# Performance work log

Hardware: AMD Instinct MI355X
Metric: run time of the kernel (lower is better)

Reference implementation:

```python
import jax, jax.numpy as jnp
import numpy as np

VOCAB = 64
H = 64
B, L = 256, 2048


def setup_inputs() -> dict:
    key = jax.random.key(0)
    ks = jax.random.split(key, 12)
    s = 0.02
    return {
        "seq":   jax.random.randint(ks[0], (B, L), 0, VOCAB),
        "embed": jax.random.normal(ks[1], (VOCAB, H), jnp.float32) * s,
        "W1":    jax.random.normal(ks[2], (H, 2 * H), jnp.float32) * s,
        "b1":    jnp.zeros((2 * H,), jnp.float32),
        "W2":    jax.random.normal(ks[3], (2 * H, H), jnp.float32) * s,
        "b2":    jnp.zeros((H,), jnp.float32),
        "gamma": jnp.ones((H,), jnp.float32),
        "beta":  jnp.zeros((H,), jnp.float32),
        "Wr":    jax.random.normal(ks[4], (H, H), jnp.float32) * s,
        "br":    jnp.zeros((H,), jnp.float32),
        "Wo":    jax.random.normal(ks[5], (H, VOCAB), jnp.float32) * s,
        "bo":    jnp.zeros((VOCAB,), jnp.float32),
    }


def _layernorm(x, gamma, beta, eps=1e-5):
    mu = x.mean(-1, keepdims=True)
    var = ((x - mu) ** 2).mean(-1, keepdims=True)
    return (x - mu) * jax.lax.rsqrt(var + eps) * gamma + beta


def _encode(seq, embed, W1, b1, W2, b2, gamma, beta):
    h = embed[seq]                                   # [B, L, H]
    ff = jax.nn.relu(h @ W1 + b1) @ W2 + b2
    return _layernorm(h + ff, gamma, beta)


def _run_memory(hidden):
    # sequential energy-gated delta-rule update of fast-weight M [B,H,H]
    Bd, Ld, Hd = hidden.shape
    M0 = jnp.zeros((Bd, Hd, Hd), hidden.dtype)

    def step(carry, k):
        M, writes = carry
        v = k                                        # k == v == hidden[:, t]
        v_pred = jnp.einsum('bij,bj->bi', M, k)
        denom = (k * k).sum(-1, keepdims=True) + 1e-6
        delta_v = v - v_pred / denom
        dM = delta_v[:, :, None] * k[:, None, :]     # outer product [B,H,H]
        E_before = -0.5 * (M * M).sum((-2, -1))
        Mn = M + dM
        E_after = -0.5 * (Mn * Mn).sum((-2, -1))
        gate = E_after < E_before                    # [B] bool
        M = jnp.where(gate[:, None, None], Mn, M)
        writes = writes + gate.sum().astype(jnp.float32)
        return (M, writes), None

    keys = jnp.swapaxes(hidden[:, :-1, :], 0, 1)     # [L-1, B, H]
    (M, writes), _ = jax.lax.scan(step, (M0, jnp.float32(0.0)), keys)
    return M, writes


def reference(seq, embed, W1, b1, W2, b2, gamma, beta, Wr, br, Wo, bo):
    hidden = _encode(seq, embed, W1, b1, W2, b2, gamma, beta)
    Bd, Ld, Hd = hidden.shape
    M, writes = _run_memory(hidden)
    write_rate = writes / jnp.float32(Bd * (Ld - 1))
    query = hidden[:, -1, :]
    ctx = jnp.einsum('bij,bj->bi', M, query)
    logits = (ctx @ Wr + br) @ Wo + bo               # [B, VOCAB]
    return logits, write_rate
```

## Files before the change

### kernel.cpp

```cpp
#include <hip/hip_runtime.h>
#include <math.h>

#define VOCAB 64
#define H 64
#define BB 256
#define LL 2048

__device__ __forceinline__ float wave_sum_dpp(float x) {
  int t;
  float r = x;
  t = __builtin_amdgcn_update_dpp(0, __float_as_int(r), 0x111, 0xf, 0xf, true); r += __int_as_float(t);
  t = __builtin_amdgcn_update_dpp(0, __float_as_int(r), 0x112, 0xf, 0xf, true); r += __int_as_float(t);
  t = __builtin_amdgcn_update_dpp(0, __float_as_int(r), 0x114, 0xf, 0xf, true); r += __int_as_float(t);
  t = __builtin_amdgcn_update_dpp(0, __float_as_int(r), 0x118, 0xf, 0xf, true); r += __int_as_float(t);
  t = __builtin_amdgcn_update_dpp(0, __float_as_int(r), 0x142, 0xf, 0xf, true); r += __int_as_float(t);
  t = __builtin_amdgcn_update_dpp(0, __float_as_int(r), 0x143, 0xf, 0xf, true); r += __int_as_float(t);
  return __int_as_float(__builtin_amdgcn_readlane(__float_as_int(r), 63));
}

__global__ __launch_bounds__(64, 1) void encode_kernel(
    const float* __restrict__ embed, const float* __restrict__ W1,
    const float* __restrict__ b1, const float* __restrict__ W2,
    const float* __restrict__ b2, const float* __restrict__ gamma,
    const float* __restrict__ beta, float* __restrict__ table,
    float* __restrict__ kkg) {
  const int c = blockIdx.x;
  const int j = threadIdx.x;
  __shared__ float hs[H];
  __shared__ float zs[2 * H];
  const float h = embed[c * H + j];
  hs[j] = h;
  __syncthreads();
  float z0 = b1[j], z1 = b1[j + H];
#pragma unroll 8
  for (int i = 0; i < H; ++i) {
    const float hi = hs[i];
    z0 = fmaf(hi, W1[i * 2 * H + j], z0);
    z1 = fmaf(hi, W1[i * 2 * H + j + H], z1);
  }
  z0 = fmaxf(z0, 0.f);
  z1 = fmaxf(z1, 0.f);
  zs[j] = z0;
  zs[j + H] = z1;
  __syncthreads();
  float ff = b2[j];
#pragma unroll 8
  for (int m = 0; m < 2 * H; ++m) ff = fmaf(zs[m], W2[m * H + j], ff);
  const float x = h + ff;
  const float mu = wave_sum_dpp(x) * (1.f / 64.f);
  const float d = x - mu;
  const float var = wave_sum_dpp(d * d) * (1.f / 64.f);
  const float y = d * (1.f / sqrtf(var + 1e-5f)) * gamma[j] + beta[j];
  table[c * H + j] = y;
  const float s2 = wave_sum_dpp(y * y);
  if (j == 0) kkg[c] = s2;
}

__global__ __launch_bounds__(64, 1) void scan_kernel(
    const int* __restrict__ seq, const float* __restrict__ table,
    const float* __restrict__ kkg, const float* __restrict__ Wr,
    const float* __restrict__ br, const float* __restrict__ Wo,
    const float* __restrict__ bo, float* __restrict__ out,
    float* __restrict__ counts) {
  const int b = blockIdx.x;
  const int lane = threadIdx.x;
  __shared__ float T[H * VOCAB];
  __shared__ float KK[VOCAB];
  __shared__ int toks[LL];
  __shared__ float xv[H];

  {
    const float4* src = (const float4*)table;
    float4* dst = (float4*)T;
#pragma unroll
    for (int q = 0; q < 16; ++q) dst[q * 64 + lane] = src[q * 64 + lane];
    KK[lane] = kkg[lane];
    const int4* ssrc = (const int4*)(seq + (long)b * LL);
    int4* sdst = (int4*)toks;
#pragma unroll
    for (int q = 0; q < 8; ++q) sdst[q * 64 + lane] = ssrc[q * 64 + lane];
  }
  __syncthreads();

  float M[H];
#pragma unroll
  for (int j = 0; j < H; ++j) M[j] = 0.f;
  float wcount = 0.f;

  int c = toks[0];
  for (int t = 0; t < LL - 1; ++t) {
    const int cnext = toks[t + 1];
    const float4* kp = (const float4*)(T + c * H);
    float kv[H];
    float vp0 = 0.f, vp1 = 0.f, vp2 = 0.f, vp3 = 0.f;
#pragma unroll
    for (int q = 0; q < 16; ++q) {
      const float4 k4 = kp[q];
      kv[4 * q + 0] = k4.x; kv[4 * q + 1] = k4.y;
      kv[4 * q + 2] = k4.z; kv[4 * q + 3] = k4.w;
      vp0 = fmaf(M[4 * q + 0], k4.x, vp0);
      vp1 = fmaf(M[4 * q + 1], k4.y, vp1);
      vp2 = fmaf(M[4 * q + 2], k4.z, vp2);
      vp3 = fmaf(M[4 * q + 3], k4.w, vp3);
    }
    const float vp = (vp0 + vp1) + (vp2 + vp3);
    const float kk = KK[c];
    const float ki = T[c * H + lane];
    const float dv = ki - vp / (kk + 1e-6f);
    const float a = dv * (2.f * vp + dv * kk);
    const float s = wave_sum_dpp(a);
    if (s > 0.f) {
#pragma unroll
      for (int j = 0; j < H; ++j) M[j] = fmaf(dv, kv[j], M[j]);
      wcount += 1.f;
    }
    c = cnext;
  }

  {
    const float4* kp = (const float4*)(T + c * H);
    float c0 = 0.f, c1 = 0.f, c2 = 0.f, c3 = 0.f;
#pragma unroll
    for (int q = 0; q < 16; ++q) {
      const float4 k4 = kp[q];
      c0 = fmaf(M[4 * q + 0], k4.x, c0);
      c1 = fmaf(M[4 * q + 1], k4.y, c1);
      c2 = fmaf(M[4 * q + 2], k4.z, c2);
      c3 = fmaf(M[4 * q + 3], k4.w, c3);
    }
    xv[lane] = (c0 + c1) + (c2 + c3);
  }
  __syncthreads();
  float t1 = br[lane];
#pragma unroll 8
  for (int i = 0; i < H; ++i) t1 = fmaf(xv[i], Wr[i * H + lane], t1);
  __syncthreads();
  xv[lane] = t1;
  __syncthreads();
  float lg = bo[lane];
#pragma unroll 8
  for (int m = 0; m < H; ++m) lg = fmaf(xv[m], Wo[m * H + lane], lg);
  out[(long)b * H + lane] = lg;
  if (lane == 0) counts[b] = wcount;
}

__global__ __launch_bounds__(256, 1) void finalize_kernel(const float* __restrict__ counts,
                                                          float* __restrict__ out) {
  const int lane = threadIdx.x;
  __shared__ float sbuf[BB];
  sbuf[lane] = counts[lane];
  __syncthreads();
  for (int off = BB / 2; off > 0; off >>= 1) {
    if (lane < off) sbuf[lane] += sbuf[lane + off];
    __syncthreads();
  }
  if (lane == 0) out[BB * H] = sbuf[0] / (float)(BB * (LL - 1));
}

extern "C" void kernel_launch(void* const* d_in, const int* in_sizes, int n_in,
                              void* d_out, int out_size, void* d_ws, size_t ws_size,
                              hipStream_t stream) {
  const int* seq      = (const int*)d_in[0];
  const float* embed  = (const float*)d_in[1];
  const float* W1     = (const float*)d_in[2];
  const float* b1     = (const float*)d_in[3];
  const float* W2     = (const float*)d_in[4];
  const float* b2     = (const float*)d_in[5];
  const float* gamma  = (const float*)d_in[6];
  const float* beta   = (const float*)d_in[7];
  const float* Wr     = (const float*)d_in[8];
  const float* br     = (const float*)d_in[9];
  const float* Wo     = (const float*)d_in[10];
  const float* bo     = (const float*)d_in[11];
  float* out = (float*)d_out;

  float* table  = (float*)d_ws;
  float* kkg    = table + VOCAB * H;
  float* counts = kkg + VOCAB;

  encode_kernel<<<VOCAB, H, 0, stream>>>(embed, W1, b1, W2, b2, gamma, beta, table, kkg);
  scan_kernel<<<BB, H, 0, stream>>>(seq, table, kkg, Wr, br, Wo, bo, out, counts);
  finalize_kernel<<<1, BB, 0, stream>>>(counts, out);
}
```

Baseline: 809.2 us.

## Fuse M update with next-step prediction and use packed fp32 FMA

The per-step loop is restructured so that the gated rank-1 update of M and the matrix-vector product for the next token's prediction happen in a single pass over the row. The next key row is loaded one step ahead. The data-dependent branch is replaced by a multiply with a zero-gated dv, and M is stored as float2 vectors so the FMAs can map to packed fp32 instructions. This removes a separate pass over M and the divergent branch, but every step now pays the update FMAs even when the gate rejects the write, and the prediction is computed from the updated M in a different summation order.

Result: faster. 724.8 us (-10.4%).

```diff
diff --git a/kernel.cpp b/kernel.cpp
--- a/kernel.cpp
+++ b/kernel.cpp
@@ -5,6 +5,8 @@
 #define H 64
 #define BB 256
 #define LL 2048
+
+typedef float v2f __attribute__((ext_vector_type(2)));
 
 __device__ __forceinline__ float wave_sum_dpp(float x) {
   int t;
@@ -82,54 +84,48 @@
   }
   __syncthreads();
 
-  float M[H];
+  v2f M2[32];
 #pragma unroll
-  for (int j = 0; j < H; ++j) M[j] = 0.f;
+  for (int r = 0; r < 32; ++r) M2[r] = (v2f){0.f, 0.f};
   float wcount = 0.f;
 
   int c = toks[0];
+  float sc = T[c * H + lane];
+  float kk = KK[c];
+  v2f vpA = (v2f){0.f, 0.f}, vpB = (v2f){0.f, 0.f};
+
   for (int t = 0; t < LL - 1; ++t) {
-    const int cnext = toks[t + 1];
-    const float4* kp = (const float4*)(T + c * H);
-    float kv[H];
-    float vp0 = 0.f, vp1 = 0.f, vp2 = 0.f, vp3 = 0.f;
+    const int cn = toks[t + 1];
+    const float4* kvp = (const float4*)(T + c * H);
+    const float4* knp = (const float4*)(T + cn * H);
+    const float scn = T[cn * H + lane];
+    const float kkn = KK[cn];
+
+    const float vp = (vpA.x + vpA.y) + (vpB.x + vpB.y);
+    const float dv = sc - vp / (kk + 1e-6f);
+    const float a = dv * (2.f * vp + dv * kk);
+    const float s = wave_sum_dpp(a);
+    const float dvg = s > 0.f ? dv : 0.f;
+    wcount += s > 0.f ? 1.f : 0.f;
+    const v2f dv2 = (v2f){dvg, dvg};
+
+    v2f nA = (v2f){0.f, 0.f}, nB = (v2f){0.f, 0.f};
 #pragma unroll
     for (int q = 0; q < 16; ++q) {
-      const float4 k4 = kp[q];
-      kv[4 * q + 0] = k4.x; kv[4 * q + 1] = k4.y;
-      kv[4 * q + 2] = k4.z; kv[4 * q + 3] = k4.w;
-      vp0 = fmaf(M[4 * q + 0], k4.x, vp0);
-      vp1 = fmaf(M[4 * q + 1], k4.y, vp1);
-      vp2 = fmaf(M[4 * q + 2], k4.z, vp2);
-      vp3 = fmaf(M[4 * q + 3], k4.w, vp3);
+      const float4 kv4 = kvp[q];
+      const float4 kn4 = knp[q];
+      const v2f kva = (v2f){kv4.x, kv4.y}, kvb = (v2f){kv4.z, kv4.w};
+      const v2f kna = (v2f){kn4.x, kn4.y}, knb = (v2f){kn4.z, kn4.w};
+      M2[2 * q]     = __builtin_elementwise_fma(dv2, kva, M2[2 * q]);
+      M2[2 * q + 1] = __builtin_elementwise_fma(dv2, kvb, M2[2 * q + 1]);
+      nA = __builtin_elementwise_fma(M2[2 * q],     kna, nA);
+      nB = __builtin_elementwise_fma(M2[2 * q + 1], knb, nB);
     }
-    const float vp = (vp0 + vp1) + (vp2 + vp3);
-    const float kk = KK[c];
-    const float ki = T[c * H + lane];
-    const float dv = ki - vp / (kk + 1e-6f);
-    const float a = dv * (2.f * vp + dv * kk);
-    const float s = wave_sum_dpp(a);
-    if (s > 0.f) {
-#pragma unroll
-      for (int j = 0; j < H; ++j) M[j] = fmaf(dv, kv[j], M[j]);
-      wcount += 1.f;
-    }
-    c = cnext;
+    vpA = nA; vpB = nB;
+    c = cn; sc = scn; kk = kkn;
   }
 
-  {
-    const float4* kp = (const float4*)(T + c * H);
-    float c0 = 0.f, c1 = 0.f, c2 = 0.f, c3 = 0.f;
-#pragma unroll
-    for (int q = 0; q < 16; ++q) {
-      const float4 k4 = kp[q];
-      c0 = fmaf(M[4 * q + 0], k4.x, c0);
-      c1 = fmaf(M[4 * q + 1], k4.y, c1);
-      c2 = fmaf(M[4 * q + 2], k4.z, c2);
-      c3 = fmaf(M[4 * q + 3], k4.w, c3);
-    }
-    xv[lane] = (c0 + c1) + (c2 + c3);
-  }
+  xv[lane] = (vpA.x + vpA.y) + (vpB.x + vpB.y);
   __syncthreads();
   float t1 = br[lane];
 #pragma unroll 8
```
